# Performance work log

Hardware: AMD Instinct MI355X
Metric: run time of the kernel (lower is better)

The kernel has to match this reference:

```python
import jax, jax.numpy as jnp
import numpy as np

D_IN = 1024
D_OUT = 1024
NUM_HEADS = 16
HEAD_DIM = D_OUT // NUM_HEADS


def setup_inputs() -> dict:
    key = jax.random.key(0)
    k1, k2, k3, k4 = jax.random.split(key, 4)
    x = jax.random.normal(k1, (2, 2048, D_IN), dtype=jnp.float32)
    # Linear weights stored torch-style [out_features, in_features]
    W_qkv = jax.random.normal(k2, (3 * D_OUT, D_IN), dtype=jnp.float32) * (1.0 / np.sqrt(D_IN))
    W_out = jax.random.normal(k3, (D_OUT, D_OUT), dtype=jnp.float32) * (1.0 / np.sqrt(D_OUT))
    b_out = jax.random.normal(k4, (D_OUT,), dtype=jnp.float32) * 0.01
    return {"x": x, "W_qkv": W_qkv, "W_out": W_out, "b_out": b_out}


def reference(x, W_qkv, W_out, b_out):
    b, s, _ = x.shape
    qkv = jnp.einsum('bsi,oi->bso', x, W_qkv)  # [b, s, 3*d_out]
    q, k, v = jnp.split(qkv, 3, axis=-1)
    def to_heads(t):
        return t.reshape(b, s, NUM_HEADS, HEAD_DIM).transpose(0, 2, 1, 3)
    q, k, v = to_heads(q), to_heads(k), to_heads(v)
    # NOTE: original module does NOT scale by 1/sqrt(head_dim)
    scores = jnp.einsum('bhqd,bhkd->bhqk', q, k)
    causal = jnp.tril(jnp.ones((s, s), dtype=bool))  # True = keep
    scores = jnp.where(causal[None, None], scores, -jnp.inf)
    attn = jax.nn.softmax(scores, axis=-1)
    ctx = jnp.einsum('bhqk,bhkd->bhqd', attn, v)
    ctx = ctx.transpose(0, 2, 1, 3).reshape(b, s, D_OUT)
    return jnp.einsum('bso,po->bsp', ctx, W_out) + b_out
```

## Files before the change

kernel.cpp:

```cpp
#include <hip/hip_runtime.h>
#include <cstdint>
#include <cstddef>


typedef __attribute__((ext_vector_type(8))) short bf16x8;
typedef __attribute__((ext_vector_type(4))) float f32x4;

#define LOG2E 1.44269504f

#define MFMA16(a, b, c) __builtin_amdgcn_mfma_f32_16x16x32_bf16((a), (b), (c), 0, 0, 0)

#define GLDS16(g, s)                                                        \
  __builtin_amdgcn_global_load_lds(                                         \
      (const __attribute__((address_space(1))) void*)(g),                   \
      (__attribute__((address_space(3))) void*)(s), 16, 0, 0)

#define ASYNC_BAR(N) asm volatile("s_waitcnt vmcnt(" #N ")\n\ts_barrier" ::: "memory")
#define BAR() asm volatile("s_barrier" ::: "memory")

#if __has_builtin(__builtin_amdgcn_exp2f)
#define EXP2F(x) __builtin_amdgcn_exp2f(x)
#else
#define EXP2F(x) exp2f(x)
#endif

static __device__ __forceinline__ unsigned short f2bf(float f) {
  unsigned int u = __builtin_bit_cast(unsigned int, f);
  u += 0x7FFFu + ((u >> 16) & 1u);
  return (unsigned short)(u >> 16);
}

static __device__ __forceinline__ unsigned int pk2bf(float a, float b) {
  const unsigned int ua = __builtin_bit_cast(unsigned int, a) + 0x8000u;
  const unsigned int ub = __builtin_bit_cast(unsigned int, b) + 0x8000u;
  return __builtin_amdgcn_perm(ub, ua, 0x07060302);
}

__global__ __launch_bounds__(256) void cast_bf16(const float* __restrict__ x,
                                                 const float* __restrict__ wq,
                                                 const float* __restrict__ wo,
                                                 unsigned short* __restrict__ xb,
                                                 unsigned short* __restrict__ wqb,
                                                 unsigned short* __restrict__ wob)
{
  const int id = blockIdx.x * 256 + threadIdx.x;
  const float* src;
  unsigned short* dst;
  int off;
  if (id < 1048576)               { src = x;  dst = xb;  off = id; }
  else if (id < 1048576 + 786432) { src = wq; dst = wqb; off = id - 1048576; }
  else                            { src = wo; dst = wob; off = id - (1048576 + 786432); }
  float4 v = ((const float4*)src)[off];
  ushort4 o;
  o.x = f2bf(v.x); o.y = f2bf(v.y); o.z = f2bf(v.z); o.w = f2bf(v.w);
  ((ushort4*)dst)[off] = o;
}

#define MMAC(AF, BF, MS, NS)                                                       \
  do {                                                                             \
    __builtin_amdgcn_s_setprio(1);                                                 \
    if (swapped) {                                                                 \
      _Pragma("unroll")                                                            \
      for (int mt = 0; mt < 4; ++mt)                                               \
        _Pragma("unroll")                                                          \
        for (int nt = 0; nt < 2; ++nt) {                                           \
          acc[(MS)*4+mt][(NS)*2+nt] = MFMA16(BF[nt][0], AF[mt][0], acc[(MS)*4+mt][(NS)*2+nt]); \
          acc[(MS)*4+mt][(NS)*2+nt] = MFMA16(BF[nt][1], AF[mt][1], acc[(MS)*4+mt][(NS)*2+nt]); \
        }                                                                          \
    } else {                                                                       \
      _Pragma("unroll")                                                            \
      for (int mt = 0; mt < 4; ++mt)                                               \
        _Pragma("unroll")                                                          \
        for (int nt = 0; nt < 2; ++nt) {                                           \
          acc[(MS)*4+mt][(NS)*2+nt] = MFMA16(AF[mt][0], BF[nt][0], acc[(MS)*4+mt][(NS)*2+nt]); \
          acc[(MS)*4+mt][(NS)*2+nt] = MFMA16(AF[mt][1], BF[nt][1], acc[(MS)*4+mt][(NS)*2+nt]); \
        }                                                                          \
    }                                                                              \
    __builtin_amdgcn_s_setprio(0);                                                 \
  } while (0)

__global__ __launch_bounds__(512, 2) void gemm_qkv(const unsigned short* __restrict__ A,
                                                   const unsigned short* __restrict__ B,
                                                   unsigned short* __restrict__ Qb,
                                                   unsigned short* __restrict__ Kb,
                                                   unsigned short* __restrict__ Vt)
{
  __shared__ unsigned short pool[65536];

  const int tid  = threadIdx.x;
  const int wave = tid >> 6, lane = tid & 63, quad = lane >> 4, cl = lane & 15;
  const int wm = wave >> 2, wn = wave & 3;

  const int bid = blockIdx.x;
  const int xcd = bid & 7, j = bid >> 3;
  const int mb = (xcd >> 1) * 4 + j / 6;
  const int nb = (xcd & 1) * 6 + j % 6;
  const int m0 = mb * 256, n0 = nb * 256;
  const int part = nb >> 2;
  const bool swapped = (part < 2);

  const int lrow = lane >> 3;
  const int sg   = (lane & 7) ^ lrow;

  auto stageA = [&](int h0, int buf, int k0) {
    #pragma unroll
    for (int ii = 0; ii < 2; ++ii) {
      const int r0 = h0 + wave * 16 + ii * 8;
      GLDS16(A + (size_t)(m0 + r0 + lrow) * 1024 + k0 + sg * 8,
             &pool[buf * 32768 + r0 * 64]);
    }
  };
  auto stageB = [&](int h0, int buf, int k0) {
    #pragma unroll
    for (int ii = 0; ii < 2; ++ii) {
      const int r0 = h0 + wave * 16 + ii * 8;
      GLDS16(B + (size_t)(n0 + r0 + lrow) * 1024 + k0 + sg * 8,
             &pool[buf * 32768 + 16384 + r0 * 64]);
    }
  };

  const int rswz = cl & 7;
  auto loadA = [&](bf16x8 (&af)[4][2], int msub, int b) {
    const unsigned short* base = &pool[b * 32768];
    #pragma unroll
    for (int mt = 0; mt < 4; ++mt) {
      const int row = wm * 128 + msub * 64 + mt * 16 + cl;
      #pragma unroll
      for (int kk = 0; kk < 2; ++kk)
        af[mt][kk] = *(const bf16x8*)&base[row * 64 + ((kk * 4 + quad) ^ rswz) * 8];
    }
  };
  auto loadB = [&](bf16x8 (&bf)[2][2], int nsub, int b) {
    const unsigned short* base = &pool[b * 32768 + 16384];
    #pragma unroll
    for (int nt = 0; nt < 2; ++nt) {
      const int row = wn * 64 + nsub * 32 + nt * 16 + cl;
      #pragma unroll
      for (int kk = 0; kk < 2; ++kk)
        bf[nt][kk] = *(const bf16x8*)&base[row * 64 + ((kk * 4 + quad) ^ rswz) * 8];
    }
  };

  f32x4 acc[8][4];
  #pragma unroll
  for (int i = 0; i < 8; ++i)
    #pragma unroll
    for (int jj = 0; jj < 4; ++jj)
      #pragma unroll
      for (int r = 0; r < 4; ++r) acc[i][jj][r] = 0.f;

  stageB(0,   0, 0);
  stageA(0,   0, 0);
  stageB(128, 0, 0);
  stageA(128, 0, 0);
  stageB(0,   1, 64);
  stageA(0,   1, 64);

  #pragma unroll 1
  for (int t = 0; t < 16; ++t) {
    const int b = t & 1, bn = b ^ 1;
    const int kc  = (t + 1) * 64;
    const int kc2 = (t + 2) * 64;

    bf16x8 af[4][2], bfA[2][2], bfB[2][2];

    if (t < 15) { ASYNC_BAR(4); } else { ASYNC_BAR(0); }
    loadA(af, 0, b);
    loadB(bfA, 0, b);
    if (t < 15) stageB(128, bn, kc);
    MMAC(af, bfA, 0, 0);

    loadB(bfB, 1, b);
    if (t < 15) stageA(128, bn, kc);
    MMAC(af, bfB, 0, 1);

    BAR();
    loadA(af, 1, b);
    if (t < 14) stageB(0, b, kc2);
    MMAC(af, bfB, 1, 1);

    BAR();
    if (t < 14) stageA(0, b, kc2);
    MMAC(af, bfA, 1, 0);
  }

  const int bb = m0 >> 11, ss = m0 & 2047;
  if (part < 2) {
    unsigned short* dst = (part == 0) ? Qb : Kb;
    const float sc2 = (part == 0) ? LOG2E : 1.0f;
    const int npb = (n0 & 1023) + wn * 64;
    #pragma unroll
    for (int mt = 0; mt < 8; ++mt) {
      const int m = ss + wm * 128 + mt * 16 + cl;
      #pragma unroll
      for (int nt = 0; nt < 4; ++nt) {
        const int np = npb + nt * 16 + quad * 4;
        const int hh = np >> 6, d0 = np & 63;
        ushort4 pk;
        pk.x = f2bf(acc[mt][nt][0] * sc2);
        pk.y = f2bf(acc[mt][nt][1] * sc2);
        pk.z = f2bf(acc[mt][nt][2] * sc2);
        pk.w = f2bf(acc[mt][nt][3] * sc2);
        *(ushort4*)&dst[((size_t)(bb * 16 + hh) * 2048 + m) * 64 + d0] = pk;
      }
    }
  } else {
    unsigned short* trans = pool;
    #pragma unroll 1
    for (int r = 0; r < 2; ++r) {
      __syncthreads();
      if ((wn >> 1) == r) {
        #pragma unroll
        for (int mt = 0; mt < 8; ++mt) {
          const int s_l = wm * 128 + mt * 16 + quad * 4;
          #pragma unroll
          for (int nt = 0; nt < 4; ++nt) {
            const int n_l = (wn & 1) * 64 + nt * 16 + cl;
            ushort4 pk;
            pk.x = f2bf(acc[mt][nt][0]); pk.y = f2bf(acc[mt][nt][1]);
            pk.z = f2bf(acc[mt][nt][2]); pk.w = f2bf(acc[mt][nt][3]);
            *(ushort4*)&trans[n_l * 264 + s_l] = pk;
          }
        }
      }
      __syncthreads();
      const int row = tid >> 2, q4 = tid & 3;
      const int nv = (n0 & 1023) + r * 128 + row;
      const int hh = nv >> 6, d = nv & 63;
      unsigned short* drow = Vt + ((size_t)(bb * 16 + hh) * 64 + d) * 2048 + ss + q4 * 64;
      #pragma unroll
      for (int i = 0; i < 8; ++i)
        *(bf16x8*)(drow + i * 8) = *(const bf16x8*)&trans[row * 264 + q4 * 64 + i * 8];
    }
  }
}

template <int MODE>
__global__ __launch_bounds__(256) void gemm_bt(const unsigned short* __restrict__ A,
                                               const unsigned short* __restrict__ B,
                                               const float* __restrict__ bias,
                                               float* __restrict__ OutF,
                                               unsigned short* __restrict__ Qb,
                                               unsigned short* __restrict__ Kb,
                                               unsigned short* __restrict__ Vt)
{
  __shared__ unsigned short pool[24576];

  const int tid  = threadIdx.x;
  const int wave = tid >> 6, lane = tid & 63, quad = lane >> 4, cl = lane & 15;
  const int wm = wave >> 1, wn = wave & 1;
  const int m0 = blockIdx.y * 128, n0 = blockIdx.x * 128;
  const int sr = lane >> 2, sc = lane & 3;

  const int part = (MODE == 1) ? (n0 >> 10) : 0;
  const bool swapped = (MODE == 0) || (part < 2);

  f32x4 acc[4][4];
  #pragma unroll
  for (int i = 0; i < 4; ++i)
    #pragma unroll
    for (int j = 0; j < 4; ++j)
      #pragma unroll
      for (int r = 0; r < 4; ++r) acc[i][j][r] = 0.f;

  const int scs = (sc ^ ((sr >> 1) & 3)) * 8;
  const int rchunk = (quad ^ ((cl >> 1) & 3)) * 8;

  auto stage = [&](int k0, int buf) {
    unsigned short* As = pool + buf * 8192;
    unsigned short* Bs = As + 4096;
    #pragma unroll
    for (int ii = 0; ii < 2; ++ii) {
      const int r = wave * 32 + ii * 16 + sr;
      GLDS16(A + (size_t)(m0 + r) * 1024 + k0 + scs, &As[(wave * 32 + ii * 16) * 32]);
      GLDS16(B + (size_t)(n0 + r) * 1024 + k0 + scs, &Bs[(wave * 32 + ii * 16) * 32]);
    }
  };

  stage(0, 0);
  stage(32, 1);
  int cur = 0;
  #pragma unroll 1
  for (int it = 0; it < 32; ++it) {
    if (it + 2 < 32) {
      ASYNC_BAR(4);
      const int bnx = (cur == 0) ? 2 : cur - 1;
      stage((it + 2) * 32, bnx);
    } else if (it + 1 < 32) {
      ASYNC_BAR(4);
    } else {
      ASYNC_BAR(0);
    }

    const unsigned short* As = pool + cur * 8192;
    const unsigned short* Bs = As + 4096;
    bf16x8 af[4], bfr[4];
    #pragma unroll
    for (int mt = 0; mt < 4; ++mt)
      af[mt] = *(const bf16x8*)&As[(wm * 64 + mt * 16 + cl) * 32 + rchunk];
    #pragma unroll
    for (int nt = 0; nt < 4; ++nt)
      bfr[nt] = *(const bf16x8*)&Bs[(wn * 64 + nt * 16 + cl) * 32 + rchunk];

    if (swapped) {
      #pragma unroll
      for (int mt = 0; mt < 4; ++mt)
        #pragma unroll
        for (int nt = 0; nt < 4; ++nt)
          acc[mt][nt] = MFMA16(bfr[nt], af[mt], acc[mt][nt]);
    } else {
      #pragma unroll
      for (int mt = 0; mt < 4; ++mt)
        #pragma unroll
        for (int nt = 0; nt < 4; ++nt)
          acc[mt][nt] = MFMA16(af[mt], bfr[nt], acc[mt][nt]);
    }
    cur = (cur == 2) ? 0 : cur + 1;
  }

  if (MODE == 1) {
    const int bb = m0 >> 11, ss = m0 & 2047;
    if (part == 2) {
      #pragma unroll
      for (int half = 0; half < 2; ++half) {
        __syncthreads();
        if (wn == half) {
          #pragma unroll
          for (int mt = 0; mt < 4; ++mt)
            #pragma unroll
            for (int nt = 0; nt < 4; ++nt) {
              const int nl = nt * 16 + cl;
              const int ml = wm * 64 + mt * 16 + quad * 4;
              ushort4 pk;
              pk.x = f2bf(acc[mt][nt][0]); pk.y = f2bf(acc[mt][nt][1]);
              pk.z = f2bf(acc[mt][nt][2]); pk.w = f2bf(acc[mt][nt][3]);
              *(ushort4*)&pool[nl * 136 + ml] = pk;
            }
        }
        __syncthreads();
        const int row = tid >> 2, q4 = tid & 3;
        const int nglob = n0 + half * 64 + row;
        const int hh = (nglob >> 6) & 15, d = nglob & 63;
        unsigned short* drow = Vt + ((size_t)(bb * 16 + hh) * 64 + d) * 2048 + ss;
        #pragma unroll
        for (int i = 0; i < 4; ++i) {
          const bf16x8 v = *(const bf16x8*)&pool[row * 136 + q4 * 32 + i * 8];
          *(bf16x8*)(drow + q4 * 32 + i * 8) = v;
        }
      }
    } else {
      unsigned short* dst = (part == 0) ? Qb : Kb;
      const float sc2 = (part == 0) ? LOG2E : 1.0f;
      #pragma unroll
      for (int mt = 0; mt < 4; ++mt) {
        const int m = ss + wm * 64 + mt * 16 + cl;
        #pragma unroll
        for (int nt = 0; nt < 4; ++nt) {
          const int np = (n0 & 1023) + wn * 64 + nt * 16 + quad * 4;
          const int hh = np >> 6, d0 = np & 63;
          ushort4 pk;
          pk.x = f2bf(acc[mt][nt][0] * sc2);
          pk.y = f2bf(acc[mt][nt][1] * sc2);
          pk.z = f2bf(acc[mt][nt][2] * sc2);
          pk.w = f2bf(acc[mt][nt][3] * sc2);
          *(ushort4*)&dst[((size_t)(bb * 16 + hh) * 2048 + m) * 64 + d0] = pk;
        }
      }
    }
  } else {
    #pragma unroll
    for (int mt = 0; mt < 4; ++mt) {
      const int m = m0 + wm * 64 + mt * 16 + cl;
      #pragma unroll
      for (int nt = 0; nt < 4; ++nt) {
        const int n = n0 + wn * 64 + nt * 16 + quad * 4;
        const float4 bv = *(const float4*)(bias + n);
        float4 o;
        o.x = acc[mt][nt][0] + bv.x; o.y = acc[mt][nt][1] + bv.y;
        o.z = acc[mt][nt][2] + bv.z; o.w = acc[mt][nt][3] + bv.w;
        *(float4*)&OutF[(size_t)m * 1024 + n] = o;
      }
    }
  }
}

__global__ __launch_bounds__(256) void attn_mfma(const unsigned short* __restrict__ Qb,
                                                 const unsigned short* __restrict__ Kb,
                                                 const unsigned short* __restrict__ Vt,
                                                 unsigned short* __restrict__ CTX)
{
  __shared__ unsigned short Ksm[2][64 * 64];
  __shared__ unsigned short Vsm[2][64 * 64];
  __shared__ unsigned short Psm[4][32 * 40];

  const int tid  = threadIdx.x;
  const int wave = tid >> 6, lane = tid & 63, quad = lane >> 4, cl = lane & 15;

  const int L  = blockIdx.x;
  const int bh = 4 * (L & 7) + ((L >> 3) & 3);
  const int b  = bh >> 4, h = bh & 15;
  const int p  = L >> 5;
  const int g  = p * 4 + wave;
  const int qlo = g * 16;
  const int qhi = (127 - g) * 16;
  const size_t base = (size_t)bh * (2048 * 64);

  bf16x8 qf[2][2];
  #pragma unroll
  for (int dk = 0; dk < 2; ++dk) {
    qf[0][dk] = *(const bf16x8*)(Qb + base + (size_t)(qlo + cl) * 64 + dk * 32 + quad * 8);
    qf[1][dk] = *(const bf16x8*)(Qb + base + (size_t)(qhi + cl) * 64 + dk * 32 + quad * 8);
  }

  f32x4 oacc[2][4];
  #pragma unroll
  for (int mf = 0; mf < 2; ++mf)
    #pragma unroll
    for (int dt = 0; dt < 4; ++dt)
      #pragma unroll
      for (int r = 0; r < 4; ++r) oacc[mf][dt][r] = 0.f;
  float lr[2][4] = {};

  bf16x8 ones;
  #pragma unroll
  for (int k = 0; k < 8; ++k) ones[k] = (short)0x3F80;

  const int lrow  = lane >> 3;
  const int lslot = (lane & 7) ^ lrow;
  const int nch = 32 - p;

  auto stageKV = [&](int j64, int buf) {
    #pragma unroll
    for (int ii = 0; ii < 2; ++ii) {
      const int r0 = wave * 16 + ii * 8;
      GLDS16(Kb + base + (size_t)(j64 + r0 + lrow) * 64 + lslot * 8, &Ksm[buf][r0 * 64]);
      GLDS16(Vt + base + (size_t)(r0 + lrow) * 2048 + j64 + lslot * 8, &Vsm[buf][r0 * 64]);
    }
  };

  stageKV(0, 0);
  #pragma unroll 1
  for (int ch = 0; ch < nch; ++ch) {
    ASYNC_BAR(0);
    if (ch + 1 < nch) stageKV((ch + 1) * 64, (ch + 1) & 1);

    const unsigned short* Kc = Ksm[ch & 1];
    const unsigned short* Vc = Vsm[ch & 1];

    const int j64 = ch * 64;
    #pragma unroll
    for (int jli = 0; jli < 2; ++jli) {
      const int jg0 = j64 + jli * 32;
      if (jg0 > qhi + 15) continue;
      const bool lowAct = (jg0 <= qlo + 15);
      const int jl = jli * 32;

      bf16x8 kf[2][2];
      #pragma unroll
      for (int jf = 0; jf < 2; ++jf)
        #pragma unroll
        for (int dk = 0; dk < 2; ++dk) {
          const int jrow = jl + jf * 16 + cl;
          const int slot = (dk * 4 + quad) ^ (cl & 7);
          kf[jf][dk] = *(const bf16x8*)&Kc[jrow * 64 + slot * 8];
        }

      f32x4 st[2][2];
      __builtin_amdgcn_s_setprio(1);
      #pragma unroll
      for (int jf = 0; jf < 2; ++jf)
        #pragma unroll
        for (int mf = 0; mf < 2; ++mf) {
          if (mf == 0 && !lowAct) continue;
          f32x4 z;
          #pragma unroll
          for (int r = 0; r < 4; ++r) z[r] = 0.f;
          z = MFMA16(kf[jf][0], qf[mf][0], z);
          st[jf][mf] = MFMA16(kf[jf][1], qf[mf][1], z);
        }
      __builtin_amdgcn_s_setprio(0);

      #pragma unroll
      for (int mf = 0; mf < 2; ++mf) {
        if (mf == 0 && !lowAct) continue;
        const int qbase = mf ? qhi : qlo;
        const bool diag = (jg0 + 32 > qbase);
        #pragma unroll
        for (int jf = 0; jf < 2; ++jf) {
          float pv[4];
          if (diag) {
            const int qg = qbase + cl;
            #pragma unroll
            for (int r = 0; r < 4; ++r) {
              const int jg = jg0 + jf * 16 + quad * 4 + r;
              pv[r] = (jg <= qg) ? EXP2F(st[jf][mf][r]) : 0.f;
            }
          } else {
            #pragma unroll
            for (int r = 0; r < 4; ++r) pv[r] = EXP2F(st[jf][mf][r]);
          }
          uint2 w;
          w.x = pk2bf(pv[0], pv[1]);
          w.y = pk2bf(pv[2], pv[3]);
          *(uint2*)&Psm[wave][(mf * 16 + cl) * 40 + jf * 16 + quad * 4] = w;
        }
      }

      bf16x8 vf[4];
      #pragma unroll
      for (int dt = 0; dt < 4; ++dt) {
        const int d = dt * 16 + cl;
        const int slot = ((jl >> 3) + quad) ^ (cl & 7);
        vf[dt] = *(const bf16x8*)&Vc[d * 64 + slot * 8];
      }

      __builtin_amdgcn_s_setprio(1);
      #pragma unroll
      for (int mf = 0; mf < 2; ++mf) {
        if (mf == 0 && !lowAct) continue;
        const bf16x8 pf = *(const bf16x8*)&Psm[wave][(mf * 16 + cl) * 40 + quad * 8];
        f32x4 z;
        #pragma unroll
        for (int r = 0; r < 4; ++r) z[r] = 0.f;
        const f32x4 ls = MFMA16(pf, ones, z);
        #pragma unroll
        for (int r = 0; r < 4; ++r) lr[mf][r] += ls[r];
        #pragma unroll
        for (int dt = 0; dt < 4; ++dt)
          oacc[mf][dt] = MFMA16(pf, vf[dt], oacc[mf][dt]);
      }
      __builtin_amdgcn_s_setprio(0);
    }
  }

  #pragma unroll
  for (int mf = 0; mf < 2; ++mf) {
    const int qbase = mf ? qhi : qlo;
    float inv[4];
    #pragma unroll
    for (int r = 0; r < 4; ++r) inv[r] = 1.f / lr[mf][r];
    #pragma unroll
    for (int dt = 0; dt < 4; ++dt)
      #pragma unroll
      for (int r = 0; r < 4; ++r)
        CTX[(size_t)(b * 2048 + qbase + quad * 4 + r) * 1024 +
            h * 64 + dt * 16 + cl] = f2bf(oacc[mf][dt][r] * inv[r]);
  }
}

extern "C" void kernel_launch(void* const* d_in, const int* in_sizes, int n_in,
                              void* d_out, int out_size, void* d_ws, size_t ws_size,
                              hipStream_t stream)
{
  const float* x    = (const float*)d_in[0];
  const float* Wqkv = (const float*)d_in[1];
  const float* Wout = (const float*)d_in[2];
  const float* bout = (const float*)d_in[3];
  float* out = (float*)d_out;

  char* ws = (char*)d_ws;
  unsigned short* xb  = (unsigned short*)(ws);
  unsigned short* wqb = (unsigned short*)(ws + 8388608);
  unsigned short* wob = (unsigned short*)(ws + 14680064);
  unsigned short* Qb  = (unsigned short*)(ws + 16777216);
  unsigned short* Kb  = (unsigned short*)(ws + 25165824);
  unsigned short* Vt  = (unsigned short*)(ws + 33554432);
  unsigned short* CTX = (unsigned short*)(ws + 41943040);

  cast_bf16<<<dim3(8192), dim3(256), 0, stream>>>(x, Wqkv, Wout, xb, wqb, wob);

  gemm_qkv<<<dim3(192), dim3(512), 0, stream>>>(xb, wqb, Qb, Kb, Vt);

  attn_mfma<<<dim3(512), dim3(256), 0, stream>>>(Qb, Kb, Vt, CTX);

  gemm_bt<0><<<dim3(8, 32), dim3(256), 0, stream>>>(CTX, wob, bout, out, nullptr, nullptr, nullptr);
}
```

Before: 187.3 us.

## Load K/V fragments directly from global into registers with double buffering

Removes the LDS staging of K and V tiles (async global-to-LDS loads plus barriers). Each wave now loads its own K and V MFMA fragments straight from global memory into two register sets that alternate between chunks, and launch bounds request two blocks per CU. This removes block-wide barriers and LDS traffic, but each wave now re-reads K/V from global/L2 (four times the global traffic per block) and register pressure rises, which may limit occupancy.

```diff
diff --git a/kernel.cpp b/kernel.cpp
--- a/kernel.cpp
+++ b/kernel.cpp
@@ -384,13 +384,11 @@
   }
 }
 
-__global__ __launch_bounds__(256) void attn_mfma(const unsigned short* __restrict__ Qb,
-                                                 const unsigned short* __restrict__ Kb,
-                                                 const unsigned short* __restrict__ Vt,
-                                                 unsigned short* __restrict__ CTX)
+__global__ __launch_bounds__(256, 2) void attn_mfma(const unsigned short* __restrict__ Qb,
+                                                    const unsigned short* __restrict__ Kb,
+                                                    const unsigned short* __restrict__ Vt,
+                                                    unsigned short* __restrict__ CTX)
 {
-  __shared__ unsigned short Ksm[2][64 * 64];
-  __shared__ unsigned short Vsm[2][64 * 64];
   __shared__ unsigned short Psm[4][32 * 40];
 
   const int tid  = threadIdx.x;
@@ -405,6 +403,9 @@
   const int qhi = (127 - g) * 16;
   const size_t base = (size_t)bh * (2048 * 64);
 
+  const unsigned short* Kbh = Kb + base;
+  const unsigned short* Vbh = Vt + base;
+
   bf16x8 qf[2][2];
   #pragma unroll
   for (int dk = 0; dk < 2; ++dk) {
@@ -425,45 +426,34 @@
   #pragma unroll
   for (int k = 0; k < 8; ++k) ones[k] = (short)0x3F80;
 
-  const int lrow  = lane >> 3;
-  const int lslot = (lane & 7) ^ lrow;
   const int nch = 32 - p;
 
-  auto stageKV = [&](int j64, int buf) {
-    #pragma unroll
-    for (int ii = 0; ii < 2; ++ii) {
-      const int r0 = wave * 16 + ii * 8;
-      GLDS16(Kb + base + (size_t)(j64 + r0 + lrow) * 64 + lslot * 8, &Ksm[buf][r0 * 64]);
-      GLDS16(Vt + base + (size_t)(r0 + lrow) * 2048 + j64 + lslot * 8, &Vsm[buf][r0 * 64]);
-    }
-  };
-
-  stageKV(0, 0);
-  #pragma unroll 1
-  for (int ch = 0; ch < nch; ++ch) {
-    ASYNC_BAR(0);
-    if (ch + 1 < nch) stageKV((ch + 1) * 64, (ch + 1) & 1);
-
-    const unsigned short* Kc = Ksm[ch & 1];
-    const unsigned short* Vc = Vsm[ch & 1];
-
+  auto loadK = [&](bf16x8 (&kf)[2][2][2], int j64) {
+    #pragma unroll
+    for (int jli = 0; jli < 2; ++jli)
+      #pragma unroll
+      for (int jf = 0; jf < 2; ++jf)
+        #pragma unroll
+        for (int dk = 0; dk < 2; ++dk)
+          kf[jli][jf][dk] = *(const bf16x8*)(
+              Kbh + (size_t)(j64 + jli * 32 + jf * 16 + cl) * 64 + dk * 32 + quad * 8);
+  };
+  auto loadV = [&](bf16x8 (&vf)[2][4], int j64) {
+    #pragma unroll
+    for (int jli = 0; jli < 2; ++jli)
+      #pragma unroll
+      for (int dt = 0; dt < 4; ++dt)
+        vf[jli][dt] = *(const bf16x8*)(
+            Vbh + (size_t)(dt * 16 + cl) * 2048 + j64 + jli * 32 + quad * 8);
+  };
+
+  auto compute = [&](const bf16x8 (&kf)[2][2][2], const bf16x8 (&vf)[2][4], int ch) {
     const int j64 = ch * 64;
     #pragma unroll
     for (int jli = 0; jli < 2; ++jli) {
       const int jg0 = j64 + jli * 32;
       if (jg0 > qhi + 15) continue;
       const bool lowAct = (jg0 <= qlo + 15);
-      const int jl = jli * 32;
-
-      bf16x8 kf[2][2];
-      #pragma unroll
-      for (int jf = 0; jf < 2; ++jf)
-        #pragma unroll
-        for (int dk = 0; dk < 2; ++dk) {
-          const int jrow = jl + jf * 16 + cl;
-          const int slot = (dk * 4 + quad) ^ (cl & 7);
-          kf[jf][dk] = *(const bf16x8*)&Kc[jrow * 64 + slot * 8];
-        }
 
       f32x4 st[2][2];
       __builtin_amdgcn_s_setprio(1);
@@ -475,8 +465,8 @@
           f32x4 z;
           #pragma unroll
           for (int r = 0; r < 4; ++r) z[r] = 0.f;
-          z = MFMA16(kf[jf][0], qf[mf][0], z);
-          st[jf][mf] = MFMA16(kf[jf][1], qf[mf][1], z);
+          z = MFMA16(kf[jli][jf][0], qf[mf][0], z);
+          st[jf][mf] = MFMA16(kf[jli][jf][1], qf[mf][1], z);
         }
       __builtin_amdgcn_s_setprio(0);
 
@@ -506,14 +496,6 @@
         }
       }
 
-      bf16x8 vf[4];
-      #pragma unroll
-      for (int dt = 0; dt < 4; ++dt) {
-        const int d = dt * 16 + cl;
-        const int slot = ((jl >> 3) + quad) ^ (cl & 7);
-        vf[dt] = *(const bf16x8*)&Vc[d * 64 + slot * 8];
-      }
-
       __builtin_amdgcn_s_setprio(1);
       #pragma unroll
       for (int mf = 0; mf < 2; ++mf) {
@@ -527,9 +509,22 @@
         for (int r = 0; r < 4; ++r) lr[mf][r] += ls[r];
         #pragma unroll
         for (int dt = 0; dt < 4; ++dt)
-          oacc[mf][dt] = MFMA16(pf, vf[dt], oacc[mf][dt]);
+          oacc[mf][dt] = MFMA16(pf, vf[jli][dt], oacc[mf][dt]);
       }
       __builtin_amdgcn_s_setprio(0);
+    }
+  };
+
+  bf16x8 kfA[2][2][2], vfA[2][4], kfB[2][2][2], vfB[2][4];
+  loadK(kfA, 0);
+  loadV(vfA, 0);
+  #pragma unroll 1
+  for (int ch = 0; ch < nch; ch += 2) {
+    if (ch + 1 < nch) { loadK(kfB, (ch + 1) * 64); loadV(vfB, (ch + 1) * 64); }
+    compute(kfA, vfA, ch);
+    if (ch + 1 < nch) {
+      if (ch + 2 < nch) { loadK(kfA, (ch + 2) * 64); loadV(vfA, (ch + 2) * 64); }
+      compute(kfB, vfB, ch + 1);
     }
   }
 
```

After: 246.0 us. 31.4% more time.

## Replace paired low/high query tiles with one tile per wave, heaviest blocks first

Applied to the files above, without the earlier changes.

The attention kernel used to pair a low and a high 16-row query tile in each wave to balance causal work. Now each wave handles a single 16-row tile, the grid doubles to 1024 blocks, and blocks are numbered so those with the most KV chunks launch first. This cuts per-wave registers and LDS and adds parallelism, but the KV tiles staged in LDS are shared by fewer query rows, so K/V traffic per unit of work goes up.

```diff
diff --git a/kernel.cpp b/kernel.cpp
--- a/kernel.cpp
+++ b/kernel.cpp
@@ -391,7 +391,7 @@
 {
   __shared__ unsigned short Ksm[2][64 * 64];
   __shared__ unsigned short Vsm[2][64 * 64];
-  __shared__ unsigned short Psm[4][32 * 40];
+  __shared__ unsigned short Psm[4][16 * 40];
 
   const int tid  = threadIdx.x;
   const int wave = tid >> 6, lane = tid & 63, quad = lane >> 4, cl = lane & 15;
@@ -399,27 +399,22 @@
   const int L  = blockIdx.x;
   const int bh = 4 * (L & 7) + ((L >> 3) & 3);
   const int b  = bh >> 4, h = bh & 15;
-  const int p  = L >> 5;
-  const int g  = p * 4 + wave;
-  const int qlo = g * 16;
-  const int qhi = (127 - g) * 16;
+  const int pp = 31 - (L >> 5);
+  const int G  = pp * 4 + wave;
+  const int qb = G * 16;
   const size_t base = (size_t)bh * (2048 * 64);
 
-  bf16x8 qf[2][2];
+  bf16x8 qf[2];
   #pragma unroll
-  for (int dk = 0; dk < 2; ++dk) {
-    qf[0][dk] = *(const bf16x8*)(Qb + base + (size_t)(qlo + cl) * 64 + dk * 32 + quad * 8);
-    qf[1][dk] = *(const bf16x8*)(Qb + base + (size_t)(qhi + cl) * 64 + dk * 32 + quad * 8);
-  }
-
-  f32x4 oacc[2][4];
+  for (int dk = 0; dk < 2; ++dk)
+    qf[dk] = *(const bf16x8*)(Qb + base + (size_t)(qb + cl) * 64 + dk * 32 + quad * 8);
+
+  f32x4 oacc[4];
   #pragma unroll
-  for (int mf = 0; mf < 2; ++mf)
-    #pragma unroll
-    for (int dt = 0; dt < 4; ++dt)
-      #pragma unroll
-      for (int r = 0; r < 4; ++r) oacc[mf][dt][r] = 0.f;
-  float lr[2][4] = {};
+  for (int dt = 0; dt < 4; ++dt)
+    #pragma unroll
+    for (int r = 0; r < 4; ++r) oacc[dt][r] = 0.f;
+  float lr[4] = {};
 
   bf16x8 ones;
   #pragma unroll
@@ -427,7 +422,7 @@
 
   const int lrow  = lane >> 3;
   const int lslot = (lane & 7) ^ lrow;
-  const int nch = 32 - p;
+  const int nch = pp + 1;
 
   auto stageKV = [&](int j64, int buf) {
     #pragma unroll
@@ -451,8 +446,7 @@
     #pragma unroll
     for (int jli = 0; jli < 2; ++jli) {
       const int jg0 = j64 + jli * 32;
-      if (jg0 > qhi + 15) continue;
-      const bool lowAct = (jg0 <= qlo + 15);
+      if (jg0 > qb + 15) continue;
       const int jl = jli * 32;
 
       bf16x8 kf[2][2];
@@ -465,45 +459,37 @@
           kf[jf][dk] = *(const bf16x8*)&Kc[jrow * 64 + slot * 8];
         }
 
-      f32x4 st[2][2];
+      f32x4 st[2];
       __builtin_amdgcn_s_setprio(1);
       #pragma unroll
-      for (int jf = 0; jf < 2; ++jf)
-        #pragma unroll
-        for (int mf = 0; mf < 2; ++mf) {
-          if (mf == 0 && !lowAct) continue;
-          f32x4 z;
+      for (int jf = 0; jf < 2; ++jf) {
+        f32x4 z;
+        #pragma unroll
+        for (int r = 0; r < 4; ++r) z[r] = 0.f;
+        z = MFMA16(kf[jf][0], qf[0], z);
+        st[jf] = MFMA16(kf[jf][1], qf[1], z);
+      }
+      __builtin_amdgcn_s_setprio(0);
+
+      const bool diag = (jg0 + 32 > qb);
+      #pragma unroll
+      for (int jf = 0; jf < 2; ++jf) {
+        float pv[4];
+        if (diag) {
+          const int qg = qb + cl;
           #pragma unroll
-          for (int r = 0; r < 4; ++r) z[r] = 0.f;
-          z = MFMA16(kf[jf][0], qf[mf][0], z);
-          st[jf][mf] = MFMA16(kf[jf][1], qf[mf][1], z);
+          for (int r = 0; r < 4; ++r) {
+            const int jg = jg0 + jf * 16 + quad * 4 + r;
+            pv[r] = (jg <= qg) ? EXP2F(st[jf][r]) : 0.f;
+          }
+        } else {
+          #pragma unroll
+          for (int r = 0; r < 4; ++r) pv[r] = EXP2F(st[jf][r]);
         }
-      __builtin_amdgcn_s_setprio(0);
-
-      #pragma unroll
-      for (int mf = 0; mf < 2; ++mf) {
-        if (mf == 0 && !lowAct) continue;
-        const int qbase = mf ? qhi : qlo;
-        const bool diag = (jg0 + 32 > qbase);
-        #pragma unroll
-        for (int jf = 0; jf < 2; ++jf) {
-          float pv[4];
-          if (diag) {
-            const int qg = qbase + cl;
-            #pragma unroll
-            for (int r = 0; r < 4; ++r) {
-              const int jg = jg0 + jf * 16 + quad * 4 + r;
-              pv[r] = (jg <= qg) ? EXP2F(st[jf][mf][r]) : 0.f;
-            }
-          } else {
-            #pragma unroll
-            for (int r = 0; r < 4; ++r) pv[r] = EXP2F(st[jf][mf][r]);
-          }
-          uint2 w;
-          w.x = pk2bf(pv[0], pv[1]);
-          w.y = pk2bf(pv[2], pv[3]);
-          *(uint2*)&Psm[wave][(mf * 16 + cl) * 40 + jf * 16 + quad * 4] = w;
-        }
+        uint2 w;
+        w.x = pk2bf(pv[0], pv[1]);
+        w.y = pk2bf(pv[2], pv[3]);
+        *(uint2*)&Psm[wave][cl * 40 + jf * 16 + quad * 4] = w;
       }
 
       bf16x8 vf[4];
@@ -515,36 +501,32 @@
       }
 
       __builtin_amdgcn_s_setprio(1);
-      #pragma unroll
-      for (int mf = 0; mf < 2; ++mf) {
-        if (mf == 0 && !lowAct) continue;
-        const bf16x8 pf = *(const bf16x8*)&Psm[wave][(mf * 16 + cl) * 40 + quad * 8];
+      {
+        const bf16x8 pf = *(const bf16x8*)&Psm[wave][cl * 40 + quad * 8];
         f32x4 z;
         #pragma unroll
         for (int r = 0; r < 4; ++r) z[r] = 0.f;
         const f32x4 ls = MFMA16(pf, ones, z);
         #pragma unroll
-        for (int r = 0; r < 4; ++r) lr[mf][r] += ls[r];
+        for (int r = 0; r < 4; ++r) lr[r] += ls[r];
         #pragma unroll
         for (int dt = 0; dt < 4; ++dt)
-          oacc[mf][dt] = MFMA16(pf, vf[dt], oacc[mf][dt]);
+          oacc[dt] = MFMA16(pf, vf[dt], oacc[dt]);
       }
       __builtin_amdgcn_s_setprio(0);
     }
   }
 
-  #pragma unroll
-  for (int mf = 0; mf < 2; ++mf) {
-    const int qbase = mf ? qhi : qlo;
+  {
     float inv[4];
     #pragma unroll
-    for (int r = 0; r < 4; ++r) inv[r] = 1.f / lr[mf][r];
+    for (int r = 0; r < 4; ++r) inv[r] = 1.f / lr[r];
     #pragma unroll
     for (int dt = 0; dt < 4; ++dt)
       #pragma unroll
       for (int r = 0; r < 4; ++r)
-        CTX[(size_t)(b * 2048 + qbase + quad * 4 + r) * 1024 +
-            h * 64 + dt * 16 + cl] = f2bf(oacc[mf][dt][r] * inv[r]);
+        CTX[(size_t)(b * 2048 + qb + quad * 4 + r) * 1024 +
+            h * 64 + dt * 16 + cl] = f2bf(oacc[dt][r] * inv[r]);
   }
 }
 
@@ -571,7 +553,7 @@
 
   gemm_qkv<<<dim3(192), dim3(512), 0, stream>>>(xb, wqb, Qb, Kb, Vt);
 
-  attn_mfma<<<dim3(512), dim3(256), 0, stream>>>(Qb, Kb, Vt, CTX);
+  attn_mfma<<<dim3(1024), dim3(256), 0, stream>>>(Qb, Kb, Vt, CTX);
 
   gemm_bt<0><<<dim3(8, 32), dim3(256), 0, stream>>>(CTX, wob, bout, out, nullptr, nullptr, nullptr);
 }
```

Measured after the change: 186.4 us. Within noise of the previous version (-0.5%).
